# Optimization experiments

Hardware: AMD Instinct MI355X
Metric: run time of the kernel (lower is better)

The kernel has to match this reference:

```python
import jax, jax.numpy as jnp
import numpy as np

GRAPH_SIZES = [864, 1728, 3456, 6912]
VERTEX_NUM = 6890
B, NZ, FC_DIM = 128, 128, 512
CH = [128, 128, 64, 32, 16]
EDGE_FACTOR = 6  # directed edges per node (triangle mesh)
LRELU = 0.2


def setup_inputs() -> dict:
    key = jax.random.key(0)
    ks = jax.random.split(key, 24)
    s = 0.02
    inp = {
        'x': jax.random.normal(ks[0], (B, NZ), jnp.float32),
        'fc_w1': s * jax.random.normal(ks[1], (NZ, FC_DIM), jnp.float32),
        'fc_b1': jnp.zeros((FC_DIM,), jnp.float32),
        'fc_w2': s * jax.random.normal(ks[2], (FC_DIM, GRAPH_SIZES[0] * CH[0]), jnp.float32),
        'fc_b2': jnp.zeros((GRAPH_SIZES[0] * CH[0],), jnp.float32),
    }
    # Chebyshev weights [K=3, C_in, C_out] per layer (+ final conv to 3)
    cio = [(CH[0], CH[1]), (CH[1], CH[2]), (CH[2], CH[3]), (CH[3], CH[4]), (CH[4], 3)]
    for i, (ci, co) in enumerate(cio):
        inp[f'W{i}'] = s * jax.random.normal(ks[3 + i], (3, ci, co), jnp.float32)
        inp[f'b{i}'] = jnp.zeros((co,), jnp.float32)
    # fixed edge lists per level
    for i, n in enumerate(GRAPH_SIZES):
        e = EDGE_FACTOR * n
        inp[f'edge{i}'] = jax.random.randint(ks[10 + i], (2, e), 0, n, dtype=jnp.int64)
    inp['perm_back'] = jax.random.randint(ks[20], (GRAPH_SIZES[-1],), 0, GRAPH_SIZES[-1], dtype=jnp.int64)
    return inp


def cheb_conv(x, edge_index, W, b, num_nodes):
    # PyG-style ChebConv with lambda_max=2: L_hat = L - I = -D^{-1/2} A D^{-1/2}
    src, dst = edge_index[0], edge_index[1]
    deg = jnp.zeros((num_nodes,), x.dtype).at[dst].add(jnp.ones(src.shape, x.dtype))
    dinv = jnp.where(deg > 0, 1.0 / jnp.sqrt(jnp.maximum(deg, 1.0)), 0.0)
    norm = -(dinv[src] * dinv[dst])  # [E]

    def prop(h):  # h: [B, N, C] -> L_hat @ h (gather + scatter-add over edges)
        msg = h[:, src, :] * norm[None, :, None]
        return jnp.zeros_like(h).at[:, dst, :].add(msg)

    Tx0 = x
    Tx1 = prop(Tx0)
    Tx2 = 2.0 * prop(Tx1) - Tx0
    out = (jnp.einsum('bnc,co->bno', Tx0, W[0])
           + jnp.einsum('bnc,co->bno', Tx1, W[1])
           + jnp.einsum('bnc,co->bno', Tx2, W[2]))
    return out + b


def lrelu(x):
    return jnp.where(x >= 0, x, LRELU * x)


def reference(x, fc_w1, fc_b1, fc_w2, fc_b2,
              W0, b0, W1, b1, W2, b2, W3, b3, W4, b4,
              edge0, edge1, edge2, edge3, perm_back):
    h = jax.nn.relu(x @ fc_w1 + fc_b1)
    h = h @ fc_w2 + fc_b2                      # dropout = identity (eval mode)
    h = h.reshape(h.shape[0], GRAPH_SIZES[0], -1)  # [B, 864, 128]
    edges = [edge0, edge1, edge2, edge3]
    Ws = [(W0, b0), (W1, b1), (W2, b2), (W3, b3)]
    for i in range(4):
        h = lrelu(cheb_conv(h, edges[i], Ws[i][0], Ws[i][1], GRAPH_SIZES[i]))
        if i < 3:
            h = jnp.repeat(h, 2, axis=1)       # Upsample(scale_factor=2) along nodes
    h = cheb_conv(h, edge3, W4, b4, GRAPH_SIZES[3])  # final conv to 3 coords
    h = h[:, perm_back, :]                      # perm_data gather
    return h[:, :VERTEX_NUM, :]
```

## Files before the change

kernel.cpp:

```cpp
#include <hip/hip_runtime.h>
#include <hip/hip_bf16.h>

#define DEVFN __device__ __forceinline__

__global__ void k_signal(float* out, float v) {
    if (threadIdx.x == 0 && blockIdx.x == 0) out[0] = v;
}

__global__ void k_detect64(const long long* __restrict__ p, int count, int* flag) {
    if (threadIdx.x == 0 && blockIdx.x == 0) {
        int ok = 1;
        for (int i = 0; i < count; i++) {
            long long v = p[i];
            if (v < 0 || v >= (1LL << 30)) { ok = 0; break; }
        }
        *flag = ok;
    }
}

__global__ __launch_bounds__(256) void k_cvt_idx(const void* __restrict__ p, int n,
                                                 const int* __restrict__ flag,
                                                 int* __restrict__ out) {
    int i = blockIdx.x * 256 + threadIdx.x;
    if (i >= n) return;
    if (*flag) out[i] = (int)((const long long*)p)[i];
    else       out[i] = ((const int*)p)[i];
}

__global__ __launch_bounds__(256) void k_fc1(const float* __restrict__ x,
                                             const float* __restrict__ w,
                                             const float* __restrict__ b,
                                             float* __restrict__ out) {
    int j = blockIdx.x * 256 + threadIdx.x;
    int m = blockIdx.y;
    float acc = b[j];
    const float* xr = x + m * 128;
    for (int k = 0; k < 128; k++)
        acc = fmaf(xr[k], w[k * 512 + j], acc);
    out[m * 512 + j] = fmaxf(acc, 0.f);
}

__global__ __launch_bounds__(256) void k_fc2_gemm3(const float* __restrict__ h1,
                                                   const float* __restrict__ w,
                                                   const float* __restrict__ bias,
                                                   float* __restrict__ out) {
    const int N = 110592, K = 512;
    constexpr int KT = 32, MT = 128, NT = 64, AST = 37;
    __shared__ float At[MT * AST];
    __shared__ float Bt[KT * NT];

    const int tid = threadIdx.x;
    const int cg = tid & 7;
    const int rg = tid >> 3;
    const int nbase = blockIdx.x * NT;
    const int c0 = cg * 8;

    float acc[4][8];
#pragma unroll
    for (int jj = 0; jj < 8; jj++) {
        float bj = bias[nbase + c0 + jj];
#pragma unroll
        for (int r = 0; r < 4; r++) acc[r][jj] = bj;
    }

    for (int k0 = 0; k0 < K; k0 += KT) {
        __syncthreads();
#pragma unroll
        for (int it = 0; it < 4; it++) {
            int idx = tid + it * 256;
            int row = idx >> 3, k4 = (idx & 7) * 4;
            float4 a = *(const float4*)(h1 + row * K + k0 + k4);
            float* dst = At + row * AST + k4;
            dst[0] = a.x; dst[1] = a.y; dst[2] = a.z; dst[3] = a.w;
        }
#pragma unroll
        for (int it = 0; it < 2; it++) {
            int idx = tid + it * 256;
            int kk = idx >> 4, c4 = (idx & 15) * 4;
            *(float4*)(Bt + kk * NT + c4) =
                *(const float4*)(w + (size_t)(k0 + kk) * N + nbase + c4);
        }
        __syncthreads();
#pragma unroll 4
        for (int k = 0; k < KT; k++) {
            float a0 = At[(rg * 4 + 0) * AST + k];
            float a1 = At[(rg * 4 + 1) * AST + k];
            float a2 = At[(rg * 4 + 2) * AST + k];
            float a3 = At[(rg * 4 + 3) * AST + k];
            float4 w0 = *(const float4*)(Bt + k * NT + c0);
            float4 w1 = *(const float4*)(Bt + k * NT + c0 + 4);
            float wv[8] = {w0.x, w0.y, w0.z, w0.w, w1.x, w1.y, w1.z, w1.w};
#pragma unroll
            for (int jj = 0; jj < 8; jj++) {
                acc[0][jj] = fmaf(a0, wv[jj], acc[0][jj]);
                acc[1][jj] = fmaf(a1, wv[jj], acc[1][jj]);
                acc[2][jj] = fmaf(a2, wv[jj], acc[2][jj]);
                acc[3][jj] = fmaf(a3, wv[jj], acc[3][jj]);
            }
        }
    }
#pragma unroll
    for (int r = 0; r < 4; r++) {
        int m = rg * 4 + r;
        float4 o0 = {acc[r][0], acc[r][1], acc[r][2], acc[r][3]};
        float4 o1 = {acc[r][4], acc[r][5], acc[r][6], acc[r][7]};
        *(float4*)(out + (size_t)m * N + nbase + c0) = o0;
        *(float4*)(out + (size_t)m * N + nbase + c0 + 4) = o1;
    }
}

__global__ __launch_bounds__(256) void k_zero_int(int* p, int n) {
    int i = blockIdx.x * 256 + threadIdx.x;
    if (i < n) p[i] = 0;
}

__global__ __launch_bounds__(256) void k_deg(const int* __restrict__ dst, int e,
                                             int* __restrict__ deg) {
    int i = blockIdx.x * 256 + threadIdx.x;
    if (i < e) atomicAdd(&deg[dst[i]], 1);
}

__global__ __launch_bounds__(256) void k_dinv(const int* __restrict__ deg,
                                              float* __restrict__ dinv, int n) {
    int i = blockIdx.x * 256 + threadIdx.x;
    if (i < n) dinv[i] = deg[i] > 0 ? 1.0f / sqrtf((float)deg[i]) : 0.0f;
}

__global__ __launch_bounds__(256) void k_scan(const int* __restrict__ deg,
                                              int* __restrict__ row_ptr, int n) {
    __shared__ int part[256];
    int tid = threadIdx.x;
    int per = (n + 255) / 256;
    int start = tid * per;
    int end = min(start + per, n);
    int s = 0;
    for (int i = start; i < end; i++) s += deg[i];
    part[tid] = s;
    __syncthreads();
    for (int off = 1; off < 256; off <<= 1) {
        int t = (tid >= off) ? part[tid - off] : 0;
        __syncthreads();
        part[tid] += t;
        __syncthreads();
    }
    int base = (tid == 0) ? 0 : part[tid - 1];
    int run = base;
    for (int i = start; i < end; i++) { row_ptr[i] = run; run += deg[i]; }
    if (tid == 255) row_ptr[n] = part[255];
}

__global__ __launch_bounds__(256) void k_fill(const int* __restrict__ src,
                                              const int* __restrict__ dst, int e,
                                              const int* __restrict__ row_ptr,
                                              int* __restrict__ cnt,
                                              const float* __restrict__ dinv,
                                              int* __restrict__ col, float* __restrict__ val) {
    int i = blockIdx.x * 256 + threadIdx.x;
    if (i >= e) return;
    int d = dst[i], s = src[i];
    int slot = row_ptr[d] + atomicAdd(&cnt[d], 1);
    col[slot] = s;
    val[slot] = -dinv[s] * dinv[d];
}

template <int CI, int MODE>
__global__ __launch_bounds__(256) void k_prop2(const float* __restrict__ h,
                                               const float* __restrict__ sub,
                                               const int* __restrict__ row_ptr,
                                               const int* __restrict__ col,
                                               const float* __restrict__ val,
                                               float* __restrict__ out, int n) {
    constexpr int C4 = CI / 4;
    constexpr int BY = 256 / C4;
    int c4 = threadIdx.x;
    int d = blockIdx.x;
    int b = blockIdx.y * BY + threadIdx.y;
    int p0 = row_ptr[d], p1 = row_ptr[d + 1];
    float4 acc = {0.f, 0.f, 0.f, 0.f};
    const float4* hb = (const float4*)h + (size_t)b * n * C4;
    for (int p = p0; p < p1; p++) {
        float vp = val[p];
        float4 hv = hb[(size_t)col[p] * C4 + c4];
        acc.x = fmaf(vp, hv.x, acc.x);
        acc.y = fmaf(vp, hv.y, acc.y);
        acc.z = fmaf(vp, hv.z, acc.z);
        acc.w = fmaf(vp, hv.w, acc.w);
    }
    size_t oi = ((size_t)b * n + d) * C4 + c4;
    if (MODE) {
        float4 s = ((const float4*)sub)[oi];
        acc.x = 2.f * acc.x - s.x;
        acc.y = 2.f * acc.y - s.y;
        acc.z = 2.f * acc.z - s.z;
        acc.w = 2.f * acc.w - s.w;
    }
    ((float4*)out)[oi] = acc;
}

template <int CI, int CO, bool REPEAT>
__global__ __launch_bounds__(256) void k_cheb_gemm3(const float* __restrict__ t0,
                                                    const float* __restrict__ t1,
                                                    const float* __restrict__ t2,
                                                    const float* __restrict__ W,
                                                    const float* __restrict__ bias,
                                                    float* __restrict__ out, int n) {
    constexpr int CGN = CO / 8;
    constexpr int MT = 1024 / CGN;
    constexpr int KT = 32, AST = 37;
    __shared__ float At[MT * AST];
    __shared__ float Wt_s[KT * CO];

    const int tid = threadIdx.x;
    const int cg = tid % CGN;
    const int rg = tid / CGN;
    const int m_base = blockIdx.x * MT;
    const int c0 = cg * 8;

    float acc[4][8];
#pragma unroll
    for (int jj = 0; jj < 8; jj++) {
        float bj = bias[c0 + jj];
#pragma unroll
        for (int r = 0; r < 4; r++) acc[r][jj] = bj;
    }

    const float* As[3] = {t0, t1, t2};
#pragma unroll 1
    for (int t = 0; t < 3; t++) {
        const float* A = As[t];
        const float* Wg = W + t * CI * CO;
#pragma unroll 1
        for (int k0 = 0; k0 < CI; k0 += KT) {
            __syncthreads();
#pragma unroll
            for (int it = 0; it < MT / 32; it++) {
                int idx = tid + it * 256;
                int row = idx >> 3, k4 = (idx & 7) * 4;
                float4 a = *(const float4*)(A + (size_t)(m_base + row) * CI + k0 + k4);
                float* dst = At + row * AST + k4;
                dst[0] = a.x; dst[1] = a.y; dst[2] = a.z; dst[3] = a.w;
            }
#pragma unroll
            for (int it = 0; it < (KT * CO) / 1024; it++) {
                int idx = tid + it * 256;
                int kk = idx / (CO / 4), c4 = (idx % (CO / 4)) * 4;
                *(float4*)(Wt_s + kk * CO + c4) =
                    *(const float4*)(Wg + (k0 + kk) * CO + c4);
            }
            __syncthreads();
#pragma unroll 4
            for (int k = 0; k < KT; k++) {
                float a0 = At[(rg * 4 + 0) * AST + k];
                float a1 = At[(rg * 4 + 1) * AST + k];
                float a2 = At[(rg * 4 + 2) * AST + k];
                float a3 = At[(rg * 4 + 3) * AST + k];
                float4 w0 = *(const float4*)(Wt_s + k * CO + c0);
                float4 w1 = *(const float4*)(Wt_s + k * CO + c0 + 4);
                float wv[8] = {w0.x, w0.y, w0.z, w0.w, w1.x, w1.y, w1.z, w1.w};
#pragma unroll
                for (int jj = 0; jj < 8; jj++) {
                    acc[0][jj] = fmaf(a0, wv[jj], acc[0][jj]);
                    acc[1][jj] = fmaf(a1, wv[jj], acc[1][jj]);
                    acc[2][jj] = fmaf(a2, wv[jj], acc[2][jj]);
                    acc[3][jj] = fmaf(a3, wv[jj], acc[3][jj]);
                }
            }
        }
    }

#pragma unroll
    for (int r = 0; r < 4; r++) {
        int m = m_base + rg * 4 + r;
#pragma unroll
        for (int jj = 0; jj < 8; jj++) {
            float v = acc[r][jj];
            acc[r][jj] = v >= 0.f ? v : 0.2f * v;
        }
        float4 o0 = {acc[r][0], acc[r][1], acc[r][2], acc[r][3]};
        float4 o1 = {acc[r][4], acc[r][5], acc[r][6], acc[r][7]};
        if (REPEAT) {
            int b = m / n, d = m - (m / n) * n;
            size_t ob = ((size_t)b * (2 * n) + 2 * d) * CO + c0;
            *(float4*)(out + ob) = o0;
            *(float4*)(out + ob + 4) = o1;
            *(float4*)(out + ob + CO) = o0;
            *(float4*)(out + ob + CO + 4) = o1;
        } else {
            *(float4*)(out + (size_t)m * CO + c0) = o0;
            *(float4*)(out + (size_t)m * CO + c0 + 4) = o1;
        }
    }
}

template <int CI, int CO>
__global__ __launch_bounds__(256) void k_cheb_gemmABC(const float* __restrict__ t0,
                                                      const float* __restrict__ W,
                                                      const float* __restrict__ bias,
                                                      float* __restrict__ outA,
                                                      float* __restrict__ outBC) {
    constexpr int CGN = CO / 8;
    constexpr int MT = 1024 / CGN;
    constexpr int KT = 32, AST = 37;
    __shared__ float At[MT * AST];
    __shared__ float Ws[3 * KT * CO];

    const int tid = threadIdx.x;
    const int cg = tid % CGN;
    const int rg = tid / CGN;
    const int m_base = blockIdx.x * MT;
    const int c0 = cg * 8;

    float acc[3][4][8] = {};

#pragma unroll 1
    for (int k0 = 0; k0 < CI; k0 += KT) {
        __syncthreads();
#pragma unroll
        for (int it = 0; it < MT / 32; it++) {
            int idx = tid + it * 256;
            int row = idx >> 3, k4 = (idx & 7) * 4;
            float4 a = *(const float4*)(t0 + (size_t)(m_base + row) * CI + k0 + k4);
            float* dst = At + row * AST + k4;
            dst[0] = a.x; dst[1] = a.y; dst[2] = a.z; dst[3] = a.w;
        }
#pragma unroll
        for (int t = 0; t < 3; t++)
#pragma unroll
            for (int it = 0; it < CO / 32; it++) {
                int idx = tid + it * 256;
                int kk = idx / (CO / 4), c4 = (idx % (CO / 4)) * 4;
                *(float4*)(Ws + t * KT * CO + kk * CO + c4) =
                    *(const float4*)(W + t * CI * CO + (size_t)(k0 + kk) * CO + c4);
            }
        __syncthreads();
#pragma unroll 2
        for (int k = 0; k < KT; k++) {
            float a0 = At[(rg * 4 + 0) * AST + k];
            float a1 = At[(rg * 4 + 1) * AST + k];
            float a2 = At[(rg * 4 + 2) * AST + k];
            float a3 = At[(rg * 4 + 3) * AST + k];
#pragma unroll
            for (int t = 0; t < 3; t++) {
                float4 w0 = *(const float4*)(Ws + t * KT * CO + k * CO + c0);
                float4 w1 = *(const float4*)(Ws + t * KT * CO + k * CO + c0 + 4);
                float wv[8] = {w0.x, w0.y, w0.z, w0.w, w1.x, w1.y, w1.z, w1.w};
#pragma unroll
                for (int jj = 0; jj < 8; jj++) {
                    acc[t][0][jj] = fmaf(a0, wv[jj], acc[t][0][jj]);
                    acc[t][1][jj] = fmaf(a1, wv[jj], acc[t][1][jj]);
                    acc[t][2][jj] = fmaf(a2, wv[jj], acc[t][2][jj]);
                    acc[t][3][jj] = fmaf(a3, wv[jj], acc[t][3][jj]);
                }
            }
        }
    }

#pragma unroll
    for (int r = 0; r < 4; r++) {
        size_t m = m_base + rg * 4 + r;
        float av[8], bv[8], cv[8];
#pragma unroll
        for (int jj = 0; jj < 8; jj++) {
            cv[jj] = acc[2][r][jj];
            av[jj] = acc[0][r][jj] - cv[jj] + bias[c0 + jj];
            bv[jj] = acc[1][r][jj];
        }
        *(float4*)(outA + m * CO + c0)     = (float4){av[0], av[1], av[2], av[3]};
        *(float4*)(outA + m * CO + c0 + 4) = (float4){av[4], av[5], av[6], av[7]};
        float* bc = outBC + m * 2 * CO;
        *(float4*)(bc + c0)          = (float4){bv[0], bv[1], bv[2], bv[3]};
        *(float4*)(bc + c0 + 4)      = (float4){bv[4], bv[5], bv[6], bv[7]};
        *(float4*)(bc + CO + c0)     = (float4){cv[0], cv[1], cv[2], cv[3]};
        *(float4*)(bc + CO + c0 + 4) = (float4){cv[4], cv[5], cv[6], cv[7]};
    }
}

__global__ __launch_bounds__(256) void k_cheb_smallABC(const float* __restrict__ t0,
                                                       const float* __restrict__ W,
                                                       const float* __restrict__ bias,
                                                       float* __restrict__ outA,
                                                       float* __restrict__ outBC) {
    constexpr int CI = 32, CO = 16, MT = 256, AST = 33;
    __shared__ float At[MT * AST];
    __shared__ float Ws[3 * CI * CO];

    const int tid = threadIdx.x;
    const int cg = tid & 1;
    const int rg = tid >> 1;
    const int c0 = cg * 8;
    const int m_base = blockIdx.x * MT;

    for (int i = tid; i < 384; i += 256)
        ((float4*)Ws)[i] = ((const float4*)W)[i];

#pragma unroll
    for (int it = 0; it < 8; it++) {
        int idx = tid + it * 256;
        int row = idx >> 3, k4 = (idx & 7) * 4;
        float4 a = *(const float4*)(t0 + (size_t)(m_base + row) * CI + k4);
        float* dst = At + row * AST + k4;
        dst[0] = a.x; dst[1] = a.y; dst[2] = a.z; dst[3] = a.w;
    }
    __syncthreads();

    float acc[3][2][8] = {};
#pragma unroll 4
    for (int k = 0; k < CI; k++) {
        float a0 = At[rg * AST + k];
        float a1 = At[(rg + 128) * AST + k];
#pragma unroll
        for (int t = 0; t < 3; t++) {
            float4 w0 = *(const float4*)(Ws + t * CI * CO + k * CO + c0);
            float4 w1 = *(const float4*)(Ws + t * CI * CO + k * CO + c0 + 4);
            float wv[8] = {w0.x, w0.y, w0.z, w0.w, w1.x, w1.y, w1.z, w1.w};
#pragma unroll
            for (int jj = 0; jj < 8; jj++) {
                acc[t][0][jj] = fmaf(a0, wv[jj], acc[t][0][jj]);
                acc[t][1][jj] = fmaf(a1, wv[jj], acc[t][1][jj]);
            }
        }
    }

#pragma unroll
    for (int r = 0; r < 2; r++) {
        size_t m = m_base + rg + r * 128;
        float av[8], bv[8], cv[8];
#pragma unroll
        for (int jj = 0; jj < 8; jj++) {
            cv[jj] = acc[2][r][jj];
            av[jj] = acc[0][r][jj] - cv[jj] + bias[c0 + jj];
            bv[jj] = acc[1][r][jj];
        }
        *(float4*)(outA + m * CO + c0)     = (float4){av[0], av[1], av[2], av[3]};
        *(float4*)(outA + m * CO + c0 + 4) = (float4){av[4], av[5], av[6], av[7]};
        float* bc = outBC + m * 2 * CO;
        *(float4*)(bc + c0)          = (float4){bv[0], bv[1], bv[2], bv[3]};
        *(float4*)(bc + c0 + 4)      = (float4){bv[4], bv[5], bv[6], bv[7]};
        *(float4*)(bc + CO + c0)     = (float4){cv[0], cv[1], cv[2], cv[3]};
        *(float4*)(bc + CO + c0 + 4) = (float4){cv[4], cv[5], cv[6], cv[7]};
    }
}

template <int CO, bool REPEAT>
__global__ __launch_bounds__(256) void k_prop_comb(const float* __restrict__ pbc,
                                                   const float* __restrict__ a,
                                                   const int* __restrict__ row_ptr,
                                                   const int* __restrict__ col,
                                                   const float* __restrict__ val,
                                                   float* __restrict__ out, int n) {
    constexpr int C4 = CO / 4;
    constexpr int BY = 256 / C4;
    int c4 = threadIdx.x;
    int d = blockIdx.x;
    int b = blockIdx.y * BY + threadIdx.y;
    int p0 = row_ptr[d], p1 = row_ptr[d + 1];
    float4 acc = {0.f, 0.f, 0.f, 0.f};
    const float4* pb4 = (const float4*)pbc + (size_t)b * n * (2 * C4);
    for (int p = p0; p < p1; p++) {
        float vp = val[p];
        float4 hv = pb4[(size_t)col[p] * (2 * C4) + C4 + c4];
        acc.x = fmaf(vp, hv.x, acc.x);
        acc.y = fmaf(vp, hv.y, acc.y);
        acc.z = fmaf(vp, hv.z, acc.z);
        acc.w = fmaf(vp, hv.w, acc.w);
    }
    size_t node = (size_t)b * n + d;
    float4 av = ((const float4*)a)[node * C4 + c4];
    float4 pbv = pb4[(size_t)d * (2 * C4) + c4];
    float4 f;
    f.x = av.x + pbv.x + 2.f * acc.x;
    f.y = av.y + pbv.y + 2.f * acc.y;
    f.z = av.z + pbv.z + 2.f * acc.z;
    f.w = av.w + pbv.w + 2.f * acc.w;
    f.x = f.x >= 0.f ? f.x : 0.2f * f.x;
    f.y = f.y >= 0.f ? f.y : 0.2f * f.y;
    f.z = f.z >= 0.f ? f.z : 0.2f * f.z;
    f.w = f.w >= 0.f ? f.w : 0.2f * f.w;
    if (REPEAT) {
        size_t o = ((size_t)b * 2 * n + 2 * d) * C4 + c4;
        ((float4*)out)[o] = f;
        ((float4*)out)[o + C4] = f;
    } else {
        ((float4*)out)[node * C4 + c4] = f;
    }
}

__global__ __launch_bounds__(256) void k_final_conv(const float* __restrict__ t0,
                                                    const float* __restrict__ t1,
                                                    const float* __restrict__ t2,
                                                    const float* __restrict__ W,
                                                    const float* __restrict__ bias,
                                                    float* __restrict__ out, int M) {
    int m = blockIdx.x * 256 + threadIdx.x;
    if (m >= M) return;
    float a0 = bias[0], a1 = bias[1], a2 = bias[2];
    const float* hs[3] = {t0, t1, t2};
#pragma unroll
    for (int t = 0; t < 3; t++) {
        const float4* h4 = (const float4*)(hs[t] + (size_t)m * 16);
        const float* Wt = W + t * 48;
#pragma unroll
        for (int q = 0; q < 4; q++) {
            float4 hv = h4[q];
            const float* Wq = Wt + q * 12;
            a0 = fmaf(hv.x, Wq[0], a0); a1 = fmaf(hv.x, Wq[1], a1); a2 = fmaf(hv.x, Wq[2], a2);
            a0 = fmaf(hv.y, Wq[3], a0); a1 = fmaf(hv.y, Wq[4], a1); a2 = fmaf(hv.y, Wq[5], a2);
            a0 = fmaf(hv.z, Wq[6], a0); a1 = fmaf(hv.z, Wq[7], a1); a2 = fmaf(hv.z, Wq[8], a2);
            a0 = fmaf(hv.w, Wq[9], a0); a1 = fmaf(hv.w, Wq[10], a1); a2 = fmaf(hv.w, Wq[11], a2);
        }
    }
    out[(size_t)m * 3 + 0] = a0;
    out[(size_t)m * 3 + 1] = a1;
    out[(size_t)m * 3 + 2] = a2;
}

__global__ __launch_bounds__(256) void k_permute(const float* __restrict__ h,
                                                 const int* __restrict__ perm,
                                                 float* __restrict__ out) {
    const int V = 6890, N = 6912;
    int idx = blockIdx.x * 256 + threadIdx.x;
    if (idx >= 128 * V * 3) return;
    int c = idx % 3;
    int t = idx / 3;
    int v = t % V;
    int b = t / V;
    int p = perm[v];
    out[idx] = h[((size_t)b * N + p) * 3 + c];
}

extern "C" void kernel_launch(void* const* d_in, const int* in_sizes, int n_in,
                              void* d_out, int out_size, void* d_ws, size_t ws_size,
                              hipStream_t stream) {
    float* out = (float*)d_out;

    static const int SIZES[20] = {
        16384, 65536, 512, 56623104, 110592,
        49152, 128, 24576, 64, 6144, 32, 1536, 16, 144, 3,
        10368, 20736, 41472, 82944, 6912
    };
    const void* in[20];
    bool map_ok = (n_in == 20);
    if (map_ok) {
        for (int s = 0; s < 20; s++) {
            int found = -1;
            for (int i = 0; i < n_in; i++)
                if (in_sizes[i] == SIZES[s]) { found = i; break; }
            if (found < 0) { map_ok = false; break; }
            in[s] = d_in[found];
        }
    }
    if (!map_ok)
        for (int i = 0; i < 20 && i < n_in; i++) in[i] = d_in[i];

    const float* x     = (const float*)in[0];
    const float* fc_w1 = (const float*)in[1];
    const float* fc_b1 = (const float*)in[2];
    const float* fc_w2 = (const float*)in[3];
    const float* fc_b2 = (const float*)in[4];
    const float* W0 = (const float*)in[5];
    const float* b0 = (const float*)in[6];
    const float* W1 = (const float*)in[7];
    const float* b1 = (const float*)in[8];
    const float* W2 = (const float*)in[9];
    const float* b2 = (const float*)in[10];
    const float* W3 = (const float*)in[11];
    const float* b3 = (const float*)in[12];
    const float* W4 = (const float*)in[13];
    const float* b4 = (const float*)in[14];

    const size_t SZ = 28311552;
    float* ws = (float*)d_ws;
    float* buf0 = ws;
    float* buf1 = ws + SZ;
    float* buf2 = ws + 2 * SZ;
    float* buf3 = ws + 3 * SZ;
    float* h1   = ws + 4 * SZ;
    float* dinv = h1 + 65536;
    float* val  = dinv + 6912;
    int* ideg = (int*)(val + 41472);
    int* rowp = ideg + 6912;
    int* cnt  = rowp + 6913;
    int* col  = cnt + 6912;
    int* e0 = col + 41472;
    int* e1 = e0 + 10368;
    int* e2 = e1 + 20736;
    int* e3 = e2 + 41472;
    int* pm = e3 + 82944;
    int* flag = pm + 6912;
    size_t needed = (char*)(flag + 1) - (char*)d_ws;
    if (ws_size < needed) {
        k_signal<<<1, 64, 0, stream>>>(out, 1000.0f);
        return;
    }

    k_detect64<<<1, 64, 0, stream>>>((const long long*)in[15], 64, flag);
    k_cvt_idx<<<(10368 + 255) / 256, 256, 0, stream>>>(in[15], 10368, flag, e0);
    k_cvt_idx<<<(20736 + 255) / 256, 256, 0, stream>>>(in[16], 20736, flag, e1);
    k_cvt_idx<<<(41472 + 255) / 256, 256, 0, stream>>>(in[17], 41472, flag, e2);
    k_cvt_idx<<<(82944 + 255) / 256, 256, 0, stream>>>(in[18], 82944, flag, e3);
    k_cvt_idx<<<(6912 + 255) / 256, 256, 0, stream>>>(in[19], 6912, flag, pm);

    k_fc1<<<dim3(2, 128), 256, 0, stream>>>(x, fc_w1, fc_b1, h1);
    k_fc2_gemm3<<<1728, 256, 0, stream>>>(h1, fc_w2, fc_b2, buf0);

    auto build = [&](const int* edge, int e, int n) {
        int nb_n = (n + 255) / 256, nb_e = (e + 255) / 256;
        k_zero_int<<<nb_n, 256, 0, stream>>>(ideg, n);
        k_zero_int<<<nb_n, 256, 0, stream>>>(cnt, n);
        k_deg<<<nb_e, 256, 0, stream>>>(edge + e, e, ideg);
        k_dinv<<<nb_n, 256, 0, stream>>>(ideg, dinv, n);
        k_scan<<<1, 256, 0, stream>>>(ideg, rowp, n);
        k_fill<<<nb_e, 256, 0, stream>>>(edge, edge + e, e, rowp, cnt, dinv, col, val);
    };

    build(e0, 6 * 864, 864);
    k_prop2<128, 0><<<dim3(864, 16), dim3(32, 8), 0, stream>>>(buf0, buf0, rowp, col, val, buf1, 864);
    k_prop2<128, 1><<<dim3(864, 16), dim3(32, 8), 0, stream>>>(buf1, buf0, rowp, col, val, buf2, 864);
    k_cheb_gemm3<128, 128, true><<<1728, 256, 0, stream>>>(buf0, buf1, buf2, W0, b0, buf3, 864);

    build(e1, 6 * 1728, 1728);
    k_cheb_gemmABC<128, 64><<<1728, 256, 0, stream>>>(buf3, W1, b1, buf1, buf2);
    k_prop2<128, 0><<<dim3(1728, 16), dim3(32, 8), 0, stream>>>(buf2, buf2, rowp, col, val, buf0, 1728);
    k_prop_comb<64, true><<<dim3(1728, 8), dim3(16, 16), 0, stream>>>(buf0, buf1, rowp, col, val, buf3, 1728);

    build(e2, 6 * 3456, 3456);
    k_cheb_gemmABC<64, 32><<<1728, 256, 0, stream>>>(buf3, W2, b2, buf1, buf2);
    k_prop2<64, 0><<<dim3(3456, 8), dim3(16, 16), 0, stream>>>(buf2, buf2, rowp, col, val, buf0, 3456);
    k_prop_comb<32, true><<<dim3(3456, 4), dim3(8, 32), 0, stream>>>(buf0, buf1, rowp, col, val, buf3, 3456);

    build(e3, 6 * 6912, 6912);
    k_cheb_smallABC<<<3456, 256, 0, stream>>>(buf3, W3, b3, buf1, buf2);
    k_prop2<32, 0><<<dim3(6912, 4), dim3(8, 32), 0, stream>>>(buf2, buf2, rowp, col, val, buf0, 6912);
    k_prop_comb<16, false><<<dim3(6912, 2), dim3(4, 64), 0, stream>>>(buf0, buf1, rowp, col, val, buf3, 6912);

    k_prop2<16, 0><<<dim3(6912, 2), dim3(4, 64), 0, stream>>>(buf3, buf3, rowp, col, val, buf1, 6912);
    k_prop2<16, 1><<<dim3(6912, 2), dim3(4, 64), 0, stream>>>(buf1, buf3, rowp, col, val, buf2, 6912);
    k_final_conv<<<(884736 + 255) / 256, 256, 0, stream>>>(buf3, buf1, buf2, W4, b4, buf0, 884736);

    int tot = 128 * 6890 * 3;
    k_permute<<<(tot + 255) / 256, 256, 0, stream>>>(buf0, pm, out);

    if (!map_ok) k_signal<<<1, 64, 0, stream>>>(out, 2000.0f);
}
```

Measured before the change: 1.962 ms.

## Skip materializing node upsampling; index half-resolution buffers via col>>1

The repeat-by-2 upsampling is no longer written out. Each later layer's per-node GEMM runs on the half-size pre-upsample tensor with half the blocks. The propagation and combine kernels then read source rows at index col>>1 and d>>1. This removes the duplicated writes and halves GEMM work for layers 1-3, but relies on the GEMM kernels working correctly with the halved grid and on the buffer layout matching the new indexing.

After: 1.729 ms. -11.9%, faster.

```diff
diff --git a/kernel.cpp b/kernel.cpp
--- a/kernel.cpp
+++ b/kernel.cpp
@@ -197,6 +197,68 @@
     ((float4*)out)[oi] = acc;
 }
 
+template <int CI>
+__global__ __launch_bounds__(256) void k_prop_bc(const float* __restrict__ src,
+                                                 const int* __restrict__ row_ptr,
+                                                 const int* __restrict__ col,
+                                                 const float* __restrict__ val,
+                                                 float* __restrict__ out, int n) {
+    constexpr int C4 = CI / 4;
+    constexpr int BY = 256 / C4;
+    int c4 = threadIdx.x;
+    int d = blockIdx.x;
+    int b = blockIdx.y * BY + threadIdx.y;
+    int p0 = row_ptr[d], p1 = row_ptr[d + 1];
+    float4 acc = {0.f, 0.f, 0.f, 0.f};
+    const float4* hb = (const float4*)src + (size_t)b * (n >> 1) * C4;
+    for (int p = p0; p < p1; p++) {
+        float vp = val[p];
+        float4 hv = hb[(size_t)(col[p] >> 1) * C4 + c4];
+        acc.x = fmaf(vp, hv.x, acc.x);
+        acc.y = fmaf(vp, hv.y, acc.y);
+        acc.z = fmaf(vp, hv.z, acc.z);
+        acc.w = fmaf(vp, hv.w, acc.w);
+    }
+    ((float4*)out)[((size_t)b * n + d) * C4 + c4] = acc;
+}
+
+template <int CO>
+__global__ __launch_bounds__(256) void k_prop_comb2(const float* __restrict__ pbc,
+                                                    const float* __restrict__ a,
+                                                    const int* __restrict__ row_ptr,
+                                                    const int* __restrict__ col,
+                                                    const float* __restrict__ val,
+                                                    float* __restrict__ out, int n) {
+    constexpr int C4 = CO / 4;
+    constexpr int BY = 256 / C4;
+    int c4 = threadIdx.x;
+    int d = blockIdx.x;
+    int b = blockIdx.y * BY + threadIdx.y;
+    int p0 = row_ptr[d], p1 = row_ptr[d + 1];
+    float4 acc = {0.f, 0.f, 0.f, 0.f};
+    const float4* pb4 = (const float4*)pbc + (size_t)b * n * (2 * C4);
+    for (int p = p0; p < p1; p++) {
+        float vp = val[p];
+        float4 hv = pb4[(size_t)col[p] * (2 * C4) + C4 + c4];
+        acc.x = fmaf(vp, hv.x, acc.x);
+        acc.y = fmaf(vp, hv.y, acc.y);
+        acc.z = fmaf(vp, hv.z, acc.z);
+        acc.w = fmaf(vp, hv.w, acc.w);
+    }
+    float4 av = ((const float4*)a)[((size_t)b * (n >> 1) + (d >> 1)) * C4 + c4];
+    float4 pbv = pb4[(size_t)d * (2 * C4) + c4];
+    float4 f;
+    f.x = av.x + pbv.x + 2.f * acc.x;
+    f.y = av.y + pbv.y + 2.f * acc.y;
+    f.z = av.z + pbv.z + 2.f * acc.z;
+    f.w = av.w + pbv.w + 2.f * acc.w;
+    f.x = f.x >= 0.f ? f.x : 0.2f * f.x;
+    f.y = f.y >= 0.f ? f.y : 0.2f * f.y;
+    f.z = f.z >= 0.f ? f.z : 0.2f * f.z;
+    f.w = f.w >= 0.f ? f.w : 0.2f * f.w;
+    ((float4*)out)[((size_t)b * n + d) * C4 + c4] = f;
+}
+
 template <int CI, int CO, bool REPEAT>
 __global__ __launch_bounds__(256) void k_cheb_gemm3(const float* __restrict__ t0,
                                                     const float* __restrict__ t1,
@@ -438,50 +500,6 @@
         *(float4*)(bc + c0 + 4)      = (float4){bv[4], bv[5], bv[6], bv[7]};
         *(float4*)(bc + CO + c0)     = (float4){cv[0], cv[1], cv[2], cv[3]};
         *(float4*)(bc + CO + c0 + 4) = (float4){cv[4], cv[5], cv[6], cv[7]};
-    }
-}
-
-template <int CO, bool REPEAT>
-__global__ __launch_bounds__(256) void k_prop_comb(const float* __restrict__ pbc,
-                                                   const float* __restrict__ a,
-                                                   const int* __restrict__ row_ptr,
-                                                   const int* __restrict__ col,
-                                                   const float* __restrict__ val,
-                                                   float* __restrict__ out, int n) {
-    constexpr int C4 = CO / 4;
-    constexpr int BY = 256 / C4;
-    int c4 = threadIdx.x;
-    int d = blockIdx.x;
-    int b = blockIdx.y * BY + threadIdx.y;
-    int p0 = row_ptr[d], p1 = row_ptr[d + 1];
-    float4 acc = {0.f, 0.f, 0.f, 0.f};
-    const float4* pb4 = (const float4*)pbc + (size_t)b * n * (2 * C4);
-    for (int p = p0; p < p1; p++) {
-        float vp = val[p];
-        float4 hv = pb4[(size_t)col[p] * (2 * C4) + C4 + c4];
-        acc.x = fmaf(vp, hv.x, acc.x);
-        acc.y = fmaf(vp, hv.y, acc.y);
-        acc.z = fmaf(vp, hv.z, acc.z);
-        acc.w = fmaf(vp, hv.w, acc.w);
-    }
-    size_t node = (size_t)b * n + d;
-    float4 av = ((const float4*)a)[node * C4 + c4];
-    float4 pbv = pb4[(size_t)d * (2 * C4) + c4];
-    float4 f;
-    f.x = av.x + pbv.x + 2.f * acc.x;
-    f.y = av.y + pbv.y + 2.f * acc.y;
-    f.z = av.z + pbv.z + 2.f * acc.z;
-    f.w = av.w + pbv.w + 2.f * acc.w;
-    f.x = f.x >= 0.f ? f.x : 0.2f * f.x;
-    f.y = f.y >= 0.f ? f.y : 0.2f * f.y;
-    f.z = f.z >= 0.f ? f.z : 0.2f * f.z;
-    f.w = f.w >= 0.f ? f.w : 0.2f * f.w;
-    if (REPEAT) {
-        size_t o = ((size_t)b * 2 * n + 2 * d) * C4 + c4;
-        ((float4*)out)[o] = f;
-        ((float4*)out)[o + C4] = f;
-    } else {
-        ((float4*)out)[node * C4 + c4] = f;
     }
 }
 
@@ -616,22 +634,22 @@
     build(e0, 6 * 864, 864);
     k_prop2<128, 0><<<dim3(864, 16), dim3(32, 8), 0, stream>>>(buf0, buf0, rowp, col, val, buf1, 864);
     k_prop2<128, 1><<<dim3(864, 16), dim3(32, 8), 0, stream>>>(buf1, buf0, rowp, col, val, buf2, 864);
-    k_cheb_gemm3<128, 128, true><<<1728, 256, 0, stream>>>(buf0, buf1, buf2, W0, b0, buf3, 864);
+    k_cheb_gemm3<128, 128, false><<<1728, 256, 0, stream>>>(buf0, buf1, buf2, W0, b0, buf3, 864);
 
     build(e1, 6 * 1728, 1728);
-    k_cheb_gemmABC<128, 64><<<1728, 256, 0, stream>>>(buf3, W1, b1, buf1, buf2);
-    k_prop2<128, 0><<<dim3(1728, 16), dim3(32, 8), 0, stream>>>(buf2, buf2, rowp, col, val, buf0, 1728);
-    k_prop_comb<64, true><<<dim3(1728, 8), dim3(16, 16), 0, stream>>>(buf0, buf1, rowp, col, val, buf3, 1728);
+    k_cheb_gemmABC<128, 64><<<864, 256, 0, stream>>>(buf3, W1, b1, buf1, buf2);
+    k_prop_bc<128><<<dim3(1728, 16), dim3(32, 8), 0, stream>>>(buf2, rowp, col, val, buf0, 1728);
+    k_prop_comb2<64><<<dim3(1728, 8), dim3(16, 16), 0, stream>>>(buf0, buf1, rowp, col, val, buf3, 1728);
 
     build(e2, 6 * 3456, 3456);
-    k_cheb_gemmABC<64, 32><<<1728, 256, 0, stream>>>(buf3, W2, b2, buf1, buf2);
-    k_prop2<64, 0><<<dim3(3456, 8), dim3(16, 16), 0, stream>>>(buf2, buf2, rowp, col, val, buf0, 3456);
-    k_prop_comb<32, true><<<dim3(3456, 4), dim3(8, 32), 0, stream>>>(buf0, buf1, rowp, col, val, buf3, 3456);
+    k_cheb_gemmABC<64, 32><<<864, 256, 0, stream>>>(buf3, W2, b2, buf1, buf2);
+    k_prop_bc<64><<<dim3(3456, 8), dim3(16, 16), 0, stream>>>(buf2, rowp, col, val, buf0, 3456);
+    k_prop_comb2<32><<<dim3(3456, 4), dim3(8, 32), 0, stream>>>(buf0, buf1, rowp, col, val, buf3, 3456);
 
     build(e3, 6 * 6912, 6912);
-    k_cheb_smallABC<<<3456, 256, 0, stream>>>(buf3, W3, b3, buf1, buf2);
-    k_prop2<32, 0><<<dim3(6912, 4), dim3(8, 32), 0, stream>>>(buf2, buf2, rowp, col, val, buf0, 6912);
-    k_prop_comb<16, false><<<dim3(6912, 2), dim3(4, 64), 0, stream>>>(buf0, buf1, rowp, col, val, buf3, 6912);
+    k_cheb_smallABC<<<1728, 256, 0, stream>>>(buf3, W3, b3, buf1, buf2);
+    k_prop_bc<32><<<dim3(6912, 4), dim3(8, 32), 0, stream>>>(buf2, rowp, col, val, buf0, 6912);
+    k_prop_comb2<16><<<dim3(6912, 2), dim3(4, 64), 0, stream>>>(buf0, buf1, rowp, col, val, buf3, 6912);
 
     k_prop2<16, 0><<<dim3(6912, 2), dim3(4, 64), 0, stream>>>(buf3, buf3, rowp, col, val, buf1, 6912);
     k_prop2<16, 1><<<dim3(6912, 2), dim3(4, 64), 0, stream>>>(buf1, buf3, rowp, col, val, buf2, 6912);
```
